# Optimization experiments

Hardware: AMD Instinct MI355X
Metric: run time of the kernel (lower is better)

The kernel has to match this reference:

```python
import jax, jax.numpy as jnp
import numpy as np

EMBED_DIM = 1024
NUM_HEADS = 16
HEAD_DIM = EMBED_DIM // NUM_HEADS
B, S = 2, 2048
BIG = 1e9  # clamp / nan_to_num saturation value from the torch module


def setup_inputs() -> dict:
    key = jax.random.key(0)
    k1, k2, k3, k4, k5 = jax.random.split(key, 5)
    sc = 1.0 / np.sqrt(EMBED_DIM)
    x = jax.random.normal(k1, (B, S, EMBED_DIM), dtype=jnp.float32)
    qkv_w = jax.random.normal(k2, (3 * EMBED_DIM, EMBED_DIM), dtype=jnp.float32) * sc
    qkv_b = jax.random.normal(k3, (3 * EMBED_DIM,), dtype=jnp.float32) * 0.01
    out_w = jax.random.normal(k4, (EMBED_DIM, EMBED_DIM), dtype=jnp.float32) * sc
    out_b = jax.random.normal(k5, (EMBED_DIM,), dtype=jnp.float32) * 0.01
    # causal mask, broadcastable to [B, H, S, S]; 0 => masked
    mask = jnp.tril(jnp.ones((S, S), dtype=jnp.int32))[None, None, :, :]
    return {"x": x, "mask": mask, "qkv_w": qkv_w, "qkv_b": qkv_b,
            "out_w": out_w, "out_b": out_b}


def reference(x, mask, qkv_w, qkv_b, out_w, out_b):
    b, s, e = x.shape
    # fused QKV projection (torch Linear: x @ W.T + b)
    qkv = x @ qkv_w.T + qkv_b                      # [B, S, 3E]
    q, k, v = jnp.split(qkv, 3, axis=-1)
    def heads(t):
        return t.reshape(b, s, NUM_HEADS, HEAD_DIM).transpose(0, 2, 1, 3)  # [B,H,S,D]
    q, k, v = heads(q), heads(k), heads(v)
    scores = jnp.einsum('bhqd,bhkd->bhqk', q, k) / np.sqrt(HEAD_DIM)
    scores = jnp.clip(scores, -BIG, BIG)
    # masked_fill(mask==0, -inf) then nan_to_num(neginf=-1e9) => masked -> -1e9
    scores = jnp.where(mask == 0, -jnp.inf, scores)
    scores = jnp.nan_to_num(scores, nan=0.0, posinf=BIG, neginf=-BIG)
    scores = scores - jnp.max(scores, axis=-1, keepdims=True)
    attn = jax.nn.softmax(scores, axis=-1) + 1e-9
    out = jnp.einsum('bhqk,bhkd->bhqd', attn, v)   # [B,H,S,D]
    out = out.transpose(0, 2, 1, 3).reshape(b, s, e)
    return out @ out_w.T + out_b
```

## Files before the change

kernel.cpp:

```cpp
#include <hip/hip_runtime.h>
#include <stdint.h>

#define B_ 2
#define H_ 16
#define S_ 2048
#define D_ 64
#define E_ 1024
#define M_ 4096
#define N3_ 3072

typedef __attribute__((ext_vector_type(8))) short bf16x8;
typedef __attribute__((ext_vector_type(4))) float f32x4;
typedef __attribute__((ext_vector_type(16))) float f32x16;
typedef __attribute__((ext_vector_type(4))) unsigned short us4;
typedef __attribute__((ext_vector_type(4))) int i32x4;

__device__ __forceinline__ unsigned short f2b(float f) {
  union { float f; unsigned int u; } v; v.f = f;
  unsigned int r = v.u + 0x7FFFu + ((v.u >> 16) & 1u);
  return (unsigned short)(r >> 16);
}

__device__ __forceinline__ void gll16(const void* g, void* l) {
  __builtin_amdgcn_global_load_lds((const __attribute__((address_space(1))) uint32_t*)g,
                                   (__attribute__((address_space(3))) uint32_t*)l, 16, 0, 0);
}

__global__ __launch_bounds__(256)
void f32_to_bf16_3(const float* __restrict__ a, const float* __restrict__ b,
                   const float* __restrict__ c,
                   unsigned short* __restrict__ oa, unsigned short* __restrict__ ob,
                   unsigned short* __restrict__ oc) {
  int i = (blockIdx.x * blockDim.x + threadIdx.x) * 4;
  const float* src; unsigned short* dst; int j;
  if (i < 4194304)      { src = a; dst = oa; j = i; }
  else if (i < 7340032) { src = b; dst = ob; j = i - 4194304; }
  else                  { src = c; dst = oc; j = i - 7340032; }
  float4 v = *(const float4*)(src + j);
  us4 o; o.x = f2b(v.x); o.y = f2b(v.y); o.z = f2b(v.z); o.w = f2b(v.w);
  *(us4*)(dst + j) = o;
}

template<int MODE>
__global__ __launch_bounds__(512)
void gemm_bt_k(const unsigned short* __restrict__ A,
               const unsigned short* __restrict__ Bw,
               const float* __restrict__ bias,
               float* __restrict__ outf,
               unsigned short* __restrict__ qo,
               unsigned short* __restrict__ ko,
               unsigned short* __restrict__ vto,
               const int K) {
  __shared__ unsigned short As[2][128 * 32];
  __shared__ unsigned short Bs[2][128 * 32];
  const int tid = threadIdx.x;
  const int wid = tid >> 6, lane = tid & 63;
  const int l4 = lane & 15, lh = lane >> 4;
  const int gx = gridDim.x;
  int id = blockIdx.y * gx + blockIdx.x;
  const int cpx = (gx * gridDim.y) >> 3;
  id = (id & 7) * cpx + (id >> 3);
  const int bm = (id / gx) << 7, bn = (id % gx) << 7;
  const int mq = wid >> 2, nq = wid & 3;
  f32x4 acc[4][2] = {};
  const int srow = lane >> 2;
  const int scolb = ((lane & 3) ^ (((lane >> 3) & 1) << 1)) << 4;
  auto STAGE = [&](int bb, int kt) {
    const int r = (wid << 4) + srow;
    gll16((const char*)A + ((size_t)(bm + r) * K + kt) * 2 + scolb, &As[bb][wid << 9]);
    gll16((const char*)Bw + ((size_t)(bn + r) * K + kt) * 2 + scolb, &Bs[bb][wid << 9]);
  };
  const int NT = K >> 5;
  STAGE(0, 0);
  STAGE(1, 32);
  asm volatile("s_waitcnt vmcnt(2)" ::: "memory");
  __builtin_amdgcn_s_barrier();
  asm volatile("" ::: "memory");
  const int ro = (l4 << 5) + ((lh ^ (((l4 >> 1) & 1) << 1)) << 3);
  for (int t = 0; t < NT; ++t) {
    const int bb = t & 1;
    bf16x8 af[4], bfr[2];
#pragma unroll
    for (int g = 0; g < 4; ++g)
      af[g] = *(const bf16x8*)&As[bb][(((mq << 2) + g) << 9) + ro];
#pragma unroll
    for (int h = 0; h < 2; ++h)
      bfr[h] = *(const bf16x8*)&Bs[bb][(((nq << 1) + h) << 9) + ro];
#pragma unroll
    for (int mg = 0; mg < 4; ++mg)
#pragma unroll
      for (int ng = 0; ng < 2; ++ng)
        acc[mg][ng] = __builtin_amdgcn_mfma_f32_16x16x32_bf16(af[mg], bfr[ng], acc[mg][ng], 0, 0, 0);
    asm volatile("s_waitcnt lgkmcnt(0)" ::: "memory");
    __builtin_amdgcn_s_barrier();
    if (t < NT - 2) {
      STAGE(bb, (t + 2) << 5);
      asm volatile("s_waitcnt vmcnt(2)" ::: "memory");
    } else {
      asm volatile("s_waitcnt vmcnt(0)" ::: "memory");
    }
    __builtin_amdgcn_s_barrier();
    asm volatile("" ::: "memory");
  }
#pragma unroll
  for (int mg = 0; mg < 4; ++mg) {
#pragma unroll
    for (int ng = 0; ng < 2; ++ng) {
      const int n = bn + (nq << 5) + (ng << 4) + l4;
      const float bv = bias[n];
      const int m0 = bm + (mq << 6) + (mg << 4) + (lh << 2);
      if (MODE == 1) {
#pragma unroll
        for (int i = 0; i < 4; ++i)
          outf[(size_t)(m0 + i) * E_ + n] = acc[mg][ng][i] + bv;
      } else {
        const int region = n >> 10;
        const int nn = n & 1023;
        const int h = nn >> 6, d = nn & 63;
        const int b = m0 >> 11, s0 = m0 & 2047;
        const int bh = (b << 4) + h;
        if (region == 2) {
          us4 pk;
#pragma unroll
          for (int i = 0; i < 4; ++i) pk[i] = f2b(acc[mg][ng][i] + bv);
          *(us4*)&vto[((size_t)bh * D_ + d) * S_ + s0] = pk;
        } else {
          unsigned short* dst = (region == 0) ? qo : ko;
          const float sc = (region == 0) ? 0.125f : 1.0f;
#pragma unroll
          for (int i = 0; i < 4; ++i)
            dst[((size_t)bh * S_ + s0 + i) * D_ + d] = f2b((acc[mg][ng][i] + bv) * sc);
        }
      }
    }
  }
}

__global__ __launch_bounds__(512)
void attn_k(const unsigned short* __restrict__ Q,
            const unsigned short* __restrict__ Kt,
            const unsigned short* __restrict__ Vt,
            unsigned short* __restrict__ O) {
  __shared__ __align__(16) char smem[32768];
  const int tid = threadIdx.x;
  const int wid = tid >> 6, lane = tid & 63;
  const int l31 = lane & 31, hi = lane >> 5, hi4 = hi << 2;
  const int bid = blockIdx.x;
  const int xcd = bid & 7, jj = bid >> 3;
  const int bh = (xcd << 2) + (jj & 3);
  const int pairq = jj >> 2;
  const int qbB = 15 - pairq;
  const int myqb = (wid < 4) ? pairq : qbB;
  const int q0w = (myqb << 7) + ((wid & 3) << 5);
  const int nt = (qbB + 1) << 1;
  const int ntaw = ((q0w + 31) >> 6) + 1;

  const char* Qb = (const char*)Q + (size_t)bh * (S_ * D_ * 2);
  const char* Kb = (const char*)Kt + (size_t)bh * (S_ * D_ * 2);
  const char* Vb = (const char*)Vt + (size_t)bh * (D_ * S_ * 2);

  bf16x8 qf[4];
#pragma unroll
  for (int st = 0; st < 4; ++st)
    qf[st] = *(const bf16x8*)(Qb + (size_t)(q0w + l31) * 128 + (st << 5) + (hi << 4));

  const int sw = wid & 3;
  const int r1 = (sw << 4) + (lane >> 3), r2 = r1 + 8;
  const int cc = lane & 7;
  const int ko1 = (r1 << 7) + ((cc ^ (r1 & 7)) << 4);
  const int ko2 = (r2 << 7) + ((cc ^ (r2 & 7)) << 4);
  const int vo1 = (r1 << 12) + ((cc ^ (r1 & 7)) << 4);
  const int vo2 = (r2 << 12) + ((cc ^ (r2 & 7)) << 4);

  f32x16 oacc[2] = {};
  float m_i = -3.0e38f, l_i = 0.0f;
  const int qg = q0w + l31;
  const int swl = l31 & 7;

  {
    char* kd = smem + (sw << 11);
    char* vd = smem + 16384 + (sw << 11);
    if (wid < 4) { gll16(Kb + ko1, kd); gll16(Kb + ko2, kd + 1024); }
    else         { gll16(Vb + vo1, vd); gll16(Vb + vo2, vd + 1024); }
  }
  __syncthreads();

  for (int t = 0; t < nt; ++t) {
    const int cur = t & 1;
    if (t + 1 < nt) {
      const int nb = cur ^ 1;
      char* kd = smem + (nb << 13) + (sw << 11);
      char* vd = smem + 16384 + (nb << 13) + (sw << 11);
      if (wid < 4) {
        gll16(Kb + (size_t)(t + 1) * 8192 + ko1, kd);
        gll16(Kb + (size_t)(t + 1) * 8192 + ko2, kd + 1024);
      } else {
        gll16(Vb + (size_t)(t + 1) * 128 + vo1, vd);
        gll16(Vb + (size_t)(t + 1) * 128 + vo2, vd + 1024);
      }
    }
    if (t < ntaw) {
      const char* Kc = smem + (cur << 13);
      const char* Vc = smem + 16384 + (cur << 13);
      f32x16 sacc[2] = {};
#pragma unroll
      for (int tt = 0; tt < 2; ++tt)
#pragma unroll
        for (int st = 0; st < 4; ++st) {
          bf16x8 kf = *(const bf16x8*)(Kc + (tt << 12) + (l31 << 7) + ((((st << 1) + hi) ^ swl) << 4));
          sacc[tt] = __builtin_amdgcn_mfma_f32_32x32x16_bf16(kf, qf[st], sacc[tt], 0, 0, 0);
        }
      if (t == ntaw - 1) {
        const int kv0 = t << 6;
#pragma unroll
        for (int tt = 0; tt < 2; ++tt)
#pragma unroll
          for (int r = 0; r < 16; ++r) {
            const int kg = kv0 + (tt << 5) + (r & 3) + ((r >> 2) << 3) + hi4;
            if (kg > qg) sacc[tt][r] = -3.0e38f;
          }
      }
      float pmax = -3.0e38f;
#pragma unroll
      for (int tt = 0; tt < 2; ++tt)
#pragma unroll
        for (int r = 0; r < 16; ++r) pmax = fmaxf(pmax, sacc[tt][r]);
      pmax = fmaxf(pmax, __shfl_xor(pmax, 32));
      if (__any(pmax > m_i + 8.0f)) {
        const float mn = fmaxf(m_i, pmax);
        const float scl = __expf(m_i - mn);
        l_i *= scl;
        m_i = mn;
#pragma unroll
        for (int r = 0; r < 16; ++r) {
          const float sr = __shfl(scl, (r & 3) + ((r >> 2) << 3) + hi4);
          oacc[0][r] *= sr;
          oacc[1][r] *= sr;
        }
      }
#pragma unroll
      for (int tt = 0; tt < 2; ++tt)
#pragma unroll
        for (int r = 0; r < 16; ++r) {
          const float p = __expf(sacc[tt][r] - m_i);
          l_i += p;
          sacc[tt][r] = p;
        }
#pragma unroll
      for (int ks = 0; ks < 4; ++ks) {
        const int tt = ks >> 1, r0 = (ks & 1) << 3;
        int w0, w1, w2, w3;
        asm("v_cvt_pk_bf16_f32 %0, %1, %2" : "=v"(w0) : "v"(sacc[tt][r0 + 0]), "v"(sacc[tt][r0 + 1]));
        asm("v_cvt_pk_bf16_f32 %0, %1, %2" : "=v"(w1) : "v"(sacc[tt][r0 + 2]), "v"(sacc[tt][r0 + 3]));
        asm("v_cvt_pk_bf16_f32 %0, %1, %2" : "=v"(w2) : "v"(sacc[tt][r0 + 4]), "v"(sacc[tt][r0 + 5]));
        asm("v_cvt_pk_bf16_f32 %0, %1, %2" : "=v"(w3) : "v"(sacc[tt][r0 + 6]), "v"(sacc[tt][r0 + 7]));
        asm("v_permlane32_swap_b32 %0, %1" : "+v"(w0), "+v"(w2));
        asm("v_permlane32_swap_b32 %0, %1" : "+v"(w1), "+v"(w3));
        union { i32x4 i; bf16x8 h; } u;
        u.i.x = w0; u.i.y = w1; u.i.z = w2; u.i.w = w3;
        const bf16x8 pa = u.h;
#pragma unroll
        for (int dt = 0; dt < 2; ++dt) {
          bf16x8 vf = *(const bf16x8*)(Vc + (dt << 12) + (l31 << 7) + ((((ks << 1) + hi) ^ swl) << 4));
          oacc[dt] = __builtin_amdgcn_mfma_f32_32x32x16_bf16(pa, vf, oacc[dt], 0, 0, 0);
        }
      }
    }
    __syncthreads();
  }

  const float ltot = l_i + __shfl_xor(l_i, 32);
  const float inv = 1.0f / ltot;
  const int b = bh >> 4, h = bh & 15;
#pragma unroll
  for (int r = 0; r < 16; ++r) {
    const int qr = (r & 3) + ((r >> 2) << 3) + hi4;
    const float ivr = __shfl(inv, qr);
    const size_t off = ((size_t)((b << 11) + q0w + qr) << 10) + (h << 6) + l31;
    O[off]      = f2b(oacc[0][r] * ivr);
    O[off + 32] = f2b(oacc[1][r] * ivr);
  }
}

extern "C" void kernel_launch(void* const* d_in, const int* in_sizes, int n_in,
                              void* d_out, int out_size, void* d_ws, size_t ws_size,
                              hipStream_t stream) {
  const float* x     = (const float*)d_in[0];
  const float* qkv_w = (const float*)d_in[2];
  const float* qkv_b = (const float*)d_in[3];
  const float* out_w = (const float*)d_in[4];
  const float* out_b = (const float*)d_in[5];

  unsigned short* ws   = (unsigned short*)d_ws;
  unsigned short* xb   = ws;
  unsigned short* wqkv = xb + (size_t)M_ * E_;
  unsigned short* wout = wqkv + (size_t)N3_ * E_;
  unsigned short* qB   = wout + (size_t)E_ * E_;
  unsigned short* kB   = qB + (size_t)32 * S_ * D_;
  unsigned short* vtB  = kB + (size_t)32 * S_ * D_;
  unsigned short* oB   = ws;

  f32_to_bf16_3<<<8192, 256, 0, stream>>>(x, qkv_w, out_w, xb, wqkv, wout);

  gemm_bt_k<0><<<dim3(N3_ / 128, M_ / 128), 512, 0, stream>>>(
      xb, wqkv, qkv_b, nullptr, qB, kB, vtB, E_);

  attn_k<<<256, 512, 0, stream>>>(qB, kB, vtB, oB);

  gemm_bt_k<1><<<dim3(E_ / 128, M_ / 128), 512, 0, stream>>>(
      oB, wout, out_b, (float*)d_out, nullptr, nullptr, nullptr, E_);
}
```

Measured before the change: 105.4 us.

## Triple-buffer K/V tiles and software-pipeline QK MFMA with softmax/PV

The attention kernel moves from double to triple LDS buffering of K/V tiles and unrolls the KV loop by two. This lets the QK^T MFMAs for tile t+1 issue while the softmax and PV work for tile t runs, and keeps two global-to-LDS loads in flight. The goal is to hide MFMA and exp latency and loads behind each other. In exchange, shared memory use rises to 48KB and a second score accumulator set adds register pressure under the 512-thread launch bound, which could cause spills.

```diff
diff --git a/kernel.cpp b/kernel.cpp
--- a/kernel.cpp
+++ b/kernel.cpp
@@ -141,7 +141,7 @@
             const unsigned short* __restrict__ Kt,
             const unsigned short* __restrict__ Vt,
             unsigned short* __restrict__ O) {
-  __shared__ __align__(16) char smem[32768];
+  __shared__ __align__(16) char smem[49152];
   const int tid = threadIdx.x;
   const int wid = tid >> 6, lane = tid & 63;
   const int l31 = lane & 31, hi = lane >> 5, hi4 = hi << 2;
@@ -177,95 +177,104 @@
   const int qg = q0w + l31;
   const int swl = l31 & 7;
 
-  {
-    char* kd = smem + (sw << 11);
-    char* vd = smem + 16384 + (sw << 11);
-    if (wid < 4) { gll16(Kb + ko1, kd); gll16(Kb + ko2, kd + 1024); }
-    else         { gll16(Vb + vo1, vd); gll16(Vb + vo2, vd + 1024); }
-  }
+  auto STAGE = [&](int b, int tk) {
+    char* kd = smem + b * 8192 + (sw << 11);
+    char* vd = smem + 24576 + b * 8192 + (sw << 11);
+    if (wid < 4) {
+      gll16(Kb + (size_t)tk * 8192 + ko1, kd);
+      gll16(Kb + (size_t)tk * 8192 + ko2, kd + 1024);
+    } else {
+      gll16(Vb + (size_t)tk * 128 + vo1, vd);
+      gll16(Vb + (size_t)tk * 128 + vo2, vd + 1024);
+    }
+  };
+
+  auto QK = [&](f32x16 (&S)[2], int b) {
+    const char* Kc = smem + b * 8192;
+    S[0] = (f32x16)0.0f; S[1] = (f32x16)0.0f;
+#pragma unroll
+    for (int tt = 0; tt < 2; ++tt)
+#pragma unroll
+      for (int st = 0; st < 4; ++st) {
+        bf16x8 kf = *(const bf16x8*)(Kc + (tt << 12) + (l31 << 7) + ((((st << 1) + hi) ^ swl) << 4));
+        S[tt] = __builtin_amdgcn_mfma_f32_32x32x16_bf16(kf, qf[st], S[tt], 0, 0, 0);
+      }
+  };
+
+  auto PROC = [&](int t, f32x16 (&S)[2]) {
+    if (t == ntaw - 1) {
+      const int kv0 = t << 6;
+#pragma unroll
+      for (int tt = 0; tt < 2; ++tt)
+#pragma unroll
+        for (int r = 0; r < 16; ++r) {
+          const int kg = kv0 + (tt << 5) + (r & 3) + ((r >> 2) << 3) + hi4;
+          if (kg > qg) S[tt][r] = -3.0e38f;
+        }
+    }
+    float pmax = -3.0e38f;
+#pragma unroll
+    for (int tt = 0; tt < 2; ++tt)
+#pragma unroll
+      for (int r = 0; r < 16; ++r) pmax = fmaxf(pmax, S[tt][r]);
+    pmax = fmaxf(pmax, __shfl_xor(pmax, 32));
+    if (__any(pmax > m_i + 8.0f)) {
+      const float mn = fmaxf(m_i, pmax);
+      const float scl = __expf(m_i - mn);
+      l_i *= scl;
+      m_i = mn;
+#pragma unroll
+      for (int r = 0; r < 16; ++r) {
+        const float sr = __shfl(scl, (r & 3) + ((r >> 2) << 3) + hi4);
+        oacc[0][r] *= sr;
+        oacc[1][r] *= sr;
+      }
+    }
+#pragma unroll
+    for (int tt = 0; tt < 2; ++tt)
+#pragma unroll
+      for (int r = 0; r < 16; ++r) {
+        const float p = __expf(S[tt][r] - m_i);
+        l_i += p;
+        S[tt][r] = p;
+      }
+    const char* Vc = smem + 24576 + (t % 3) * 8192;
+#pragma unroll
+    for (int ks = 0; ks < 4; ++ks) {
+      const int tt = ks >> 1, r0 = (ks & 1) << 3;
+      int w0, w1, w2, w3;
+      asm("v_cvt_pk_bf16_f32 %0, %1, %2" : "=v"(w0) : "v"(S[tt][r0 + 0]), "v"(S[tt][r0 + 1]));
+      asm("v_cvt_pk_bf16_f32 %0, %1, %2" : "=v"(w1) : "v"(S[tt][r0 + 2]), "v"(S[tt][r0 + 3]));
+      asm("v_cvt_pk_bf16_f32 %0, %1, %2" : "=v"(w2) : "v"(S[tt][r0 + 4]), "v"(S[tt][r0 + 5]));
+      asm("v_cvt_pk_bf16_f32 %0, %1, %2" : "=v"(w3) : "v"(S[tt][r0 + 6]), "v"(S[tt][r0 + 7]));
+      asm("v_permlane32_swap_b32 %0, %1" : "+v"(w0), "+v"(w2));
+      asm("v_permlane32_swap_b32 %0, %1" : "+v"(w1), "+v"(w3));
+      union { i32x4 i; bf16x8 h; } u;
+      u.i.x = w0; u.i.y = w1; u.i.z = w2; u.i.w = w3;
+      const bf16x8 pa = u.h;
+#pragma unroll
+      for (int dt = 0; dt < 2; ++dt) {
+        bf16x8 vf = *(const bf16x8*)(Vc + (dt << 12) + (l31 << 7) + ((((ks << 1) + hi) ^ swl) << 4));
+        oacc[dt] = __builtin_amdgcn_mfma_f32_32x32x16_bf16(pa, vf, oacc[dt], 0, 0, 0);
+      }
+    }
+  };
+
+  STAGE(0, 0);
+  STAGE(1, 1);
   __syncthreads();
 
-  for (int t = 0; t < nt; ++t) {
-    const int cur = t & 1;
-    if (t + 1 < nt) {
-      const int nb = cur ^ 1;
-      char* kd = smem + (nb << 13) + (sw << 11);
-      char* vd = smem + 16384 + (nb << 13) + (sw << 11);
-      if (wid < 4) {
-        gll16(Kb + (size_t)(t + 1) * 8192 + ko1, kd);
-        gll16(Kb + (size_t)(t + 1) * 8192 + ko2, kd + 1024);
-      } else {
-        gll16(Vb + (size_t)(t + 1) * 128 + vo1, vd);
-        gll16(Vb + (size_t)(t + 1) * 128 + vo2, vd + 1024);
-      }
-    }
-    if (t < ntaw) {
-      const char* Kc = smem + (cur << 13);
-      const char* Vc = smem + 16384 + (cur << 13);
-      f32x16 sacc[2] = {};
-#pragma unroll
-      for (int tt = 0; tt < 2; ++tt)
-#pragma unroll
-        for (int st = 0; st < 4; ++st) {
-          bf16x8 kf = *(const bf16x8*)(Kc + (tt << 12) + (l31 << 7) + ((((st << 1) + hi) ^ swl) << 4));
-          sacc[tt] = __builtin_amdgcn_mfma_f32_32x32x16_bf16(kf, qf[st], sacc[tt], 0, 0, 0);
-        }
-      if (t == ntaw - 1) {
-        const int kv0 = t << 6;
-#pragma unroll
-        for (int tt = 0; tt < 2; ++tt)
-#pragma unroll
-          for (int r = 0; r < 16; ++r) {
-            const int kg = kv0 + (tt << 5) + (r & 3) + ((r >> 2) << 3) + hi4;
-            if (kg > qg) sacc[tt][r] = -3.0e38f;
-          }
-      }
-      float pmax = -3.0e38f;
-#pragma unroll
-      for (int tt = 0; tt < 2; ++tt)
-#pragma unroll
-        for (int r = 0; r < 16; ++r) pmax = fmaxf(pmax, sacc[tt][r]);
-      pmax = fmaxf(pmax, __shfl_xor(pmax, 32));
-      if (__any(pmax > m_i + 8.0f)) {
-        const float mn = fmaxf(m_i, pmax);
-        const float scl = __expf(m_i - mn);
-        l_i *= scl;
-        m_i = mn;
-#pragma unroll
-        for (int r = 0; r < 16; ++r) {
-          const float sr = __shfl(scl, (r & 3) + ((r >> 2) << 3) + hi4);
-          oacc[0][r] *= sr;
-          oacc[1][r] *= sr;
-        }
-      }
-#pragma unroll
-      for (int tt = 0; tt < 2; ++tt)
-#pragma unroll
-        for (int r = 0; r < 16; ++r) {
-          const float p = __expf(sacc[tt][r] - m_i);
-          l_i += p;
-          sacc[tt][r] = p;
-        }
-#pragma unroll
-      for (int ks = 0; ks < 4; ++ks) {
-        const int tt = ks >> 1, r0 = (ks & 1) << 3;
-        int w0, w1, w2, w3;
-        asm("v_cvt_pk_bf16_f32 %0, %1, %2" : "=v"(w0) : "v"(sacc[tt][r0 + 0]), "v"(sacc[tt][r0 + 1]));
-        asm("v_cvt_pk_bf16_f32 %0, %1, %2" : "=v"(w1) : "v"(sacc[tt][r0 + 2]), "v"(sacc[tt][r0 + 3]));
-        asm("v_cvt_pk_bf16_f32 %0, %1, %2" : "=v"(w2) : "v"(sacc[tt][r0 + 4]), "v"(sacc[tt][r0 + 5]));
-        asm("v_cvt_pk_bf16_f32 %0, %1, %2" : "=v"(w3) : "v"(sacc[tt][r0 + 6]), "v"(sacc[tt][r0 + 7]));
-        asm("v_permlane32_swap_b32 %0, %1" : "+v"(w0), "+v"(w2));
-        asm("v_permlane32_swap_b32 %0, %1" : "+v"(w1), "+v"(w3));
-        union { i32x4 i; bf16x8 h; } u;
-        u.i.x = w0; u.i.y = w1; u.i.z = w2; u.i.w = w3;
-        const bf16x8 pa = u.h;
-#pragma unroll
-        for (int dt = 0; dt < 2; ++dt) {
-          bf16x8 vf = *(const bf16x8*)(Vc + (dt << 12) + (l31 << 7) + ((((ks << 1) + hi) ^ swl) << 4));
-          oacc[dt] = __builtin_amdgcn_mfma_f32_32x32x16_bf16(pa, vf, oacc[dt], 0, 0, 0);
-        }
-      }
-    }
+  f32x16 sA[2], sB[2];
+  QK(sA, 0);
+
+  for (int t = 0; t < nt; t += 2) {
+    if (t + 2 < nt) STAGE((t + 2) % 3, t + 2);
+    if (t + 1 < ntaw) QK(sB, (t + 1) % 3);
+    if (t < ntaw) PROC(t, sA);
+    __syncthreads();
+    if (t + 3 < nt) STAGE((t + 3) % 3, t + 3);
+    if (t + 2 < ntaw) QK(sA, (t + 2) % 3);
+    if (t + 1 < ntaw) PROC(t + 1, sB);
     __syncthreads();
   }
 
```

Result: no change. 106.6 us (+1.2%).

## Give each attention wave two query tiles sharing K/V fragments in 128-thread blocks

Applied to the files above, without the earlier changes.

The attention kernel moves from 512-thread blocks that paired a short and a long causal query block to 128-thread blocks of two waves. Each wave now owns two 32-row query tiles, 64 rows apart, and reuses every K and V LDS fragment for both tiles' MFMAs. Both waves stage K and V together into the double buffer. This is meant to halve LDS fragment reads per MFMA and give each wave more independent MFMA work to interleave. In exchange it doubles the accumulator registers per wave, lowers the waves per block, and drops the short/long pairing. Blocks now differ widely in workload, relying only on launch order (longest blocks first) to balance the causal triangle.

```diff
diff --git a/kernel.cpp b/kernel.cpp
--- a/kernel.cpp
+++ b/kernel.cpp
@@ -136,7 +136,7 @@
   }
 }
 
-__global__ __launch_bounds__(512)
+__global__ __launch_bounds__(128)
 void attn_k(const unsigned short* __restrict__ Q,
             const unsigned short* __restrict__ Kt,
             const unsigned short* __restrict__ Vt,
@@ -148,137 +148,193 @@
   const int bid = blockIdx.x;
   const int xcd = bid & 7, jj = bid >> 3;
   const int bh = (xcd << 2) + (jj & 3);
-  const int pairq = jj >> 2;
-  const int qbB = 15 - pairq;
-  const int myqb = (wid < 4) ? pairq : qbB;
-  const int q0w = (myqb << 7) + ((wid & 3) << 5);
-  const int nt = (qbB + 1) << 1;
-  const int ntaw = ((q0w + 31) >> 6) + 1;
+  const int qb = 15 - (jj >> 2);
+  const int q0A = (qb << 7) + (wid << 5);
+  const int q0B = q0A + 64;
+  const int nt  = (qb << 1) + 2;
+  const int ntA = nt - 1;
 
   const char* Qb = (const char*)Q + (size_t)bh * (S_ * D_ * 2);
   const char* Kb = (const char*)Kt + (size_t)bh * (S_ * D_ * 2);
   const char* Vb = (const char*)Vt + (size_t)bh * (D_ * S_ * 2);
 
-  bf16x8 qf[4];
-#pragma unroll
-  for (int st = 0; st < 4; ++st)
-    qf[st] = *(const bf16x8*)(Qb + (size_t)(q0w + l31) * 128 + (st << 5) + (hi << 4));
-
-  const int sw = wid & 3;
-  const int r1 = (sw << 4) + (lane >> 3), r2 = r1 + 8;
+  bf16x8 qfA[4], qfB[4];
+#pragma unroll
+  for (int st = 0; st < 4; ++st) {
+    qfA[st] = *(const bf16x8*)(Qb + (size_t)(q0A + l31) * 128 + (st << 5) + (hi << 4));
+    qfB[st] = *(const bf16x8*)(Qb + (size_t)(q0B + l31) * 128 + (st << 5) + (hi << 4));
+  }
+
   const int cc = lane & 7;
-  const int ko1 = (r1 << 7) + ((cc ^ (r1 & 7)) << 4);
-  const int ko2 = (r2 << 7) + ((cc ^ (r2 & 7)) << 4);
-  const int vo1 = (r1 << 12) + ((cc ^ (r1 & 7)) << 4);
-  const int vo2 = (r2 << 12) + ((cc ^ (r2 & 7)) << 4);
-
-  f32x16 oacc[2] = {};
-  float m_i = -3.0e38f, l_i = 0.0f;
-  const int qg = q0w + l31;
+  const int r0s = (wid << 5) + (lane >> 3);
+  int koX[4], voX[4];
+#pragma unroll
+  for (int i = 0; i < 4; ++i) {
+    const int r = r0s + (i << 3);
+    koX[i] = (r << 7) + ((cc ^ (r & 7)) << 4);
+    voX[i] = (r << 12) + ((cc ^ (r & 7)) << 4);
+  }
+  auto STAGE = [&](int b, int tk) {
+    char* kd = smem + (b << 13) + (wid << 12);
+    char* vd = smem + 16384 + (b << 13) + (wid << 12);
+#pragma unroll
+    for (int i = 0; i < 4; ++i) {
+      gll16(Kb + (size_t)tk * 8192 + koX[i], kd + (i << 10));
+      gll16(Vb + (size_t)tk * 128 + voX[i], vd + (i << 10));
+    }
+  };
+
+  f32x16 oA[2] = {}, oB[2] = {};
+  float mA = -3.0e38f, lA = 0.0f, mB = -3.0e38f, lB = 0.0f;
+  const int qgA = q0A + l31, qgB = q0B + l31;
   const int swl = l31 & 7;
 
-  {
-    char* kd = smem + (sw << 11);
-    char* vd = smem + 16384 + (sw << 11);
-    if (wid < 4) { gll16(Kb + ko1, kd); gll16(Kb + ko2, kd + 1024); }
-    else         { gll16(Vb + vo1, vd); gll16(Vb + vo2, vd + 1024); }
-  }
+  STAGE(0, 0);
   __syncthreads();
 
   for (int t = 0; t < nt; ++t) {
     const int cur = t & 1;
-    if (t + 1 < nt) {
-      const int nb = cur ^ 1;
-      char* kd = smem + (nb << 13) + (sw << 11);
-      char* vd = smem + 16384 + (nb << 13) + (sw << 11);
-      if (wid < 4) {
-        gll16(Kb + (size_t)(t + 1) * 8192 + ko1, kd);
-        gll16(Kb + (size_t)(t + 1) * 8192 + ko2, kd + 1024);
-      } else {
-        gll16(Vb + (size_t)(t + 1) * 128 + vo1, vd);
-        gll16(Vb + (size_t)(t + 1) * 128 + vo2, vd + 1024);
-      }
-    }
-    if (t < ntaw) {
-      const char* Kc = smem + (cur << 13);
-      const char* Vc = smem + 16384 + (cur << 13);
-      f32x16 sacc[2] = {};
-#pragma unroll
-      for (int tt = 0; tt < 2; ++tt)
-#pragma unroll
-        for (int st = 0; st < 4; ++st) {
-          bf16x8 kf = *(const bf16x8*)(Kc + (tt << 12) + (l31 << 7) + ((((st << 1) + hi) ^ swl) << 4));
-          sacc[tt] = __builtin_amdgcn_mfma_f32_32x32x16_bf16(kf, qf[st], sacc[tt], 0, 0, 0);
-        }
-      if (t == ntaw - 1) {
-        const int kv0 = t << 6;
-#pragma unroll
-        for (int tt = 0; tt < 2; ++tt)
-#pragma unroll
-          for (int r = 0; r < 16; ++r) {
-            const int kg = kv0 + (tt << 5) + (r & 3) + ((r >> 2) << 3) + hi4;
-            if (kg > qg) sacc[tt][r] = -3.0e38f;
-          }
-      }
+    if (t + 1 < nt) STAGE(cur ^ 1, t + 1);
+    const char* Kc = smem + (cur << 13);
+    const char* Vc = smem + 16384 + (cur << 13);
+    const bool aA = (t < ntA);
+    f32x16 sA[2] = {}, sB[2] = {};
+#pragma unroll
+    for (int tt = 0; tt < 2; ++tt)
+#pragma unroll
+      for (int st = 0; st < 4; ++st) {
+        bf16x8 kf = *(const bf16x8*)(Kc + (tt << 12) + (l31 << 7) + ((((st << 1) + hi) ^ swl) << 4));
+        sA[tt] = __builtin_amdgcn_mfma_f32_32x32x16_bf16(kf, qfA[st], sA[tt], 0, 0, 0);
+        sB[tt] = __builtin_amdgcn_mfma_f32_32x32x16_bf16(kf, qfB[st], sB[tt], 0, 0, 0);
+      }
+    if (t == ntA - 1) {
+      const int kv0 = t << 6;
+#pragma unroll
+      for (int tt = 0; tt < 2; ++tt)
+#pragma unroll
+        for (int r = 0; r < 16; ++r) {
+          const int kg = kv0 + (tt << 5) + (r & 3) + ((r >> 2) << 3) + hi4;
+          if (kg > qgA) sA[tt][r] = -3.0e38f;
+        }
+    }
+    if (t == nt - 1) {
+      const int kv0 = t << 6;
+#pragma unroll
+      for (int tt = 0; tt < 2; ++tt)
+#pragma unroll
+        for (int r = 0; r < 16; ++r) {
+          const int kg = kv0 + (tt << 5) + (r & 3) + ((r >> 2) << 3) + hi4;
+          if (kg > qgB) sB[tt][r] = -3.0e38f;
+        }
+    }
+    if (aA) {
       float pmax = -3.0e38f;
 #pragma unroll
       for (int tt = 0; tt < 2; ++tt)
 #pragma unroll
-        for (int r = 0; r < 16; ++r) pmax = fmaxf(pmax, sacc[tt][r]);
+        for (int r = 0; r < 16; ++r) pmax = fmaxf(pmax, sA[tt][r]);
       pmax = fmaxf(pmax, __shfl_xor(pmax, 32));
-      if (__any(pmax > m_i + 8.0f)) {
-        const float mn = fmaxf(m_i, pmax);
-        const float scl = __expf(m_i - mn);
-        l_i *= scl;
-        m_i = mn;
+      if (__any(pmax > mA + 8.0f)) {
+        const float mn = fmaxf(mA, pmax);
+        const float scl = __expf(mA - mn);
+        lA *= scl;
+        mA = mn;
 #pragma unroll
         for (int r = 0; r < 16; ++r) {
           const float sr = __shfl(scl, (r & 3) + ((r >> 2) << 3) + hi4);
-          oacc[0][r] *= sr;
-          oacc[1][r] *= sr;
-        }
-      }
-#pragma unroll
-      for (int tt = 0; tt < 2; ++tt)
-#pragma unroll
-        for (int r = 0; r < 16; ++r) {
-          const float p = __expf(sacc[tt][r] - m_i);
-          l_i += p;
-          sacc[tt][r] = p;
-        }
-#pragma unroll
-      for (int ks = 0; ks < 4; ++ks) {
-        const int tt = ks >> 1, r0 = (ks & 1) << 3;
+          oA[0][r] *= sr;
+          oA[1][r] *= sr;
+        }
+      }
+#pragma unroll
+      for (int tt = 0; tt < 2; ++tt)
+#pragma unroll
+        for (int r = 0; r < 16; ++r) {
+          const float p = __expf(sA[tt][r] - mA);
+          lA += p;
+          sA[tt][r] = p;
+        }
+    }
+    {
+      float pmax = -3.0e38f;
+#pragma unroll
+      for (int tt = 0; tt < 2; ++tt)
+#pragma unroll
+        for (int r = 0; r < 16; ++r) pmax = fmaxf(pmax, sB[tt][r]);
+      pmax = fmaxf(pmax, __shfl_xor(pmax, 32));
+      if (__any(pmax > mB + 8.0f)) {
+        const float mn = fmaxf(mB, pmax);
+        const float scl = __expf(mB - mn);
+        lB *= scl;
+        mB = mn;
+#pragma unroll
+        for (int r = 0; r < 16; ++r) {
+          const float sr = __shfl(scl, (r & 3) + ((r >> 2) << 3) + hi4);
+          oB[0][r] *= sr;
+          oB[1][r] *= sr;
+        }
+      }
+#pragma unroll
+      for (int tt = 0; tt < 2; ++tt)
+#pragma unroll
+        for (int r = 0; r < 16; ++r) {
+          const float p = __expf(sB[tt][r] - mB);
+          lB += p;
+          sB[tt][r] = p;
+        }
+    }
+#pragma unroll
+    for (int ks = 0; ks < 4; ++ks) {
+      const int tt = ks >> 1, r0 = (ks & 1) << 3;
+      bf16x8 paA, paB;
+      if (aA) {
         int w0, w1, w2, w3;
-        asm("v_cvt_pk_bf16_f32 %0, %1, %2" : "=v"(w0) : "v"(sacc[tt][r0 + 0]), "v"(sacc[tt][r0 + 1]));
-        asm("v_cvt_pk_bf16_f32 %0, %1, %2" : "=v"(w1) : "v"(sacc[tt][r0 + 2]), "v"(sacc[tt][r0 + 3]));
-        asm("v_cvt_pk_bf16_f32 %0, %1, %2" : "=v"(w2) : "v"(sacc[tt][r0 + 4]), "v"(sacc[tt][r0 + 5]));
-        asm("v_cvt_pk_bf16_f32 %0, %1, %2" : "=v"(w3) : "v"(sacc[tt][r0 + 6]), "v"(sacc[tt][r0 + 7]));
+        asm("v_cvt_pk_bf16_f32 %0, %1, %2" : "=v"(w0) : "v"(sA[tt][r0 + 0]), "v"(sA[tt][r0 + 1]));
+        asm("v_cvt_pk_bf16_f32 %0, %1, %2" : "=v"(w1) : "v"(sA[tt][r0 + 2]), "v"(sA[tt][r0 + 3]));
+        asm("v_cvt_pk_bf16_f32 %0, %1, %2" : "=v"(w2) : "v"(sA[tt][r0 + 4]), "v"(sA[tt][r0 + 5]));
+        asm("v_cvt_pk_bf16_f32 %0, %1, %2" : "=v"(w3) : "v"(sA[tt][r0 + 6]), "v"(sA[tt][r0 + 7]));
         asm("v_permlane32_swap_b32 %0, %1" : "+v"(w0), "+v"(w2));
         asm("v_permlane32_swap_b32 %0, %1" : "+v"(w1), "+v"(w3));
         union { i32x4 i; bf16x8 h; } u;
         u.i.x = w0; u.i.y = w1; u.i.z = w2; u.i.w = w3;
-        const bf16x8 pa = u.h;
-#pragma unroll
-        for (int dt = 0; dt < 2; ++dt) {
-          bf16x8 vf = *(const bf16x8*)(Vc + (dt << 12) + (l31 << 7) + ((((ks << 1) + hi) ^ swl) << 4));
-          oacc[dt] = __builtin_amdgcn_mfma_f32_32x32x16_bf16(pa, vf, oacc[dt], 0, 0, 0);
-        }
+        paA = u.h;
+      }
+      {
+        int w0, w1, w2, w3;
+        asm("v_cvt_pk_bf16_f32 %0, %1, %2" : "=v"(w0) : "v"(sB[tt][r0 + 0]), "v"(sB[tt][r0 + 1]));
+        asm("v_cvt_pk_bf16_f32 %0, %1, %2" : "=v"(w1) : "v"(sB[tt][r0 + 2]), "v"(sB[tt][r0 + 3]));
+        asm("v_cvt_pk_bf16_f32 %0, %1, %2" : "=v"(w2) : "v"(sB[tt][r0 + 4]), "v"(sB[tt][r0 + 5]));
+        asm("v_cvt_pk_bf16_f32 %0, %1, %2" : "=v"(w3) : "v"(sB[tt][r0 + 6]), "v"(sB[tt][r0 + 7]));
+        asm("v_permlane32_swap_b32 %0, %1" : "+v"(w0), "+v"(w2));
+        asm("v_permlane32_swap_b32 %0, %1" : "+v"(w1), "+v"(w3));
+        union { i32x4 i; bf16x8 h; } u;
+        u.i.x = w0; u.i.y = w1; u.i.z = w2; u.i.w = w3;
+        paB = u.h;
+      }
+#pragma unroll
+      for (int dt = 0; dt < 2; ++dt) {
+        bf16x8 vf = *(const bf16x8*)(Vc + (dt << 12) + (l31 << 7) + ((((ks << 1) + hi) ^ swl) << 4));
+        if (aA) oA[dt] = __builtin_amdgcn_mfma_f32_32x32x16_bf16(paA, vf, oA[dt], 0, 0, 0);
+        oB[dt] = __builtin_amdgcn_mfma_f32_32x32x16_bf16(paB, vf, oB[dt], 0, 0, 0);
       }
     }
     __syncthreads();
   }
 
-  const float ltot = l_i + __shfl_xor(l_i, 32);
-  const float inv = 1.0f / ltot;
+  const float ltA = lA + __shfl_xor(lA, 32);
+  const float ltB = lB + __shfl_xor(lB, 32);
+  const float invA = 1.0f / ltA, invB = 1.0f / ltB;
   const int b = bh >> 4, h = bh & 15;
 #pragma unroll
   for (int r = 0; r < 16; ++r) {
     const int qr = (r & 3) + ((r >> 2) << 3) + hi4;
-    const float ivr = __shfl(inv, qr);
-    const size_t off = ((size_t)((b << 11) + q0w + qr) << 10) + (h << 6) + l31;
-    O[off]      = f2b(oacc[0][r] * ivr);
-    O[off + 32] = f2b(oacc[1][r] * ivr);
+    const float ivA = __shfl(invA, qr), ivB = __shfl(invB, qr);
+    const size_t offA = ((size_t)((b << 11) + q0A + qr) << 10) + (h << 6) + l31;
+    const size_t offB = ((size_t)((b << 11) + q0B + qr) << 10) + (h << 6) + l31;
+    O[offA]      = f2b(oA[0][r] * ivA);
+    O[offA + 32] = f2b(oA[1][r] * ivA);
+    O[offB]      = f2b(oB[0][r] * ivB);
+    O[offB + 32] = f2b(oB[1][r] * ivB);
   }
 }
 
@@ -305,7 +361,7 @@
   gemm_bt_k<0><<<dim3(N3_ / 128, M_ / 128), 512, 0, stream>>>(
       xb, wqkv, qkv_b, nullptr, qB, kB, vtB, E_);
 
-  attn_k<<<256, 512, 0, stream>>>(qB, kB, vtB, oB);
+  attn_k<<<512, 128, 0, stream>>>(qB, kB, vtB, oB);
 
   gemm_bt_k<1><<<dim3(E_ / 128, M_ / 128), 512, 0, stream>>>(
       oB, wout, out_b, (float*)d_out, nullptr, nullptr, nullptr, E_);
```

New measurement: 166.0 us. +57.5%, slower.
